# Performance work log

Hardware: AMD Instinct MI355X
Metric: run time of the kernel (lower is better)

Reference implementation:

```python
import jax, jax.numpy as jnp
import numpy as np

N_HEAD = 16
ROPE_BASE = 10000.0


def setup_inputs() -> dict:
    key = jax.random.key(0)
    ks = jax.random.split(key, 5)
    B, T, C = 4, 1024, 2048
    s_in = 1.0 / np.sqrt(C)
    return {
        "x": jax.random.normal(ks[0], (B, T, C), dtype=jnp.float32),
        "w_attn": jax.random.normal(ks[1], (C, 3 * C), dtype=jnp.float32) * s_in,
        "b_attn": jax.random.normal(ks[2], (3 * C,), dtype=jnp.float32) * 0.01,
        "w_proj": jax.random.normal(ks[3], (C, C), dtype=jnp.float32) * s_in,
        "b_proj": jax.random.normal(ks[4], (C,), dtype=jnp.float32) * 0.01,
    }


def _rope(x, cos, sin):
    # x: (B, T, H, D); cos/sin: (T, D//2) -> broadcast over B, H
    d2 = x.shape[-1] // 2
    x1, x2 = x[..., :d2], x[..., d2:]
    c = cos[None, :, None, :]
    s = sin[None, :, None, :]
    return jnp.concatenate([x1 * c - x2 * s, x1 * s + x2 * c], axis=-1)


def reference(x, w_attn, b_attn, w_proj, b_proj):
    B, T, C = x.shape
    H = N_HEAD
    D = C // H
    qkv = (x @ w_attn + b_attn).reshape(B, T, 3, H, D)
    q, k, v = qkv[:, :, 0], qkv[:, :, 1], qkv[:, :, 2]  # (B, T, H, D)

    # Rotary embedding (GPT-NeoX / rotate-half style, full head dim)
    inv_freq = 1.0 / (ROPE_BASE ** (jnp.arange(0, D, 2, dtype=jnp.float32) / D))
    freqs = jnp.arange(T, dtype=jnp.float32)[:, None] * inv_freq[None, :]  # (T, D//2)
    cos, sin = jnp.cos(freqs), jnp.sin(freqs)
    q = _rope(q, cos, sin)
    k = _rope(k, cos, sin)

    scale = 1.0 / jnp.sqrt(jnp.asarray(D, dtype=x.dtype))
    att = jnp.einsum("bqhd,bkhd->bhqk", q, k) * scale  # (B, H, T, T)
    causal = jnp.tril(jnp.ones((T, T), dtype=bool))
    att = jnp.where(causal[None, None], att, jnp.asarray(-jnp.inf, dtype=att.dtype))
    att = jax.nn.softmax(att, axis=-1)
    y = jnp.einsum("bhqk,bkhd->bqhd", att, v).reshape(B, T, C)
    return y @ w_proj + b_proj
```

## Files before the change

kernel.cpp:

```cpp
#include <hip/hip_runtime.h>
#include <math.h>

#define T_SEQ 1024
#define C_DIM 2048
#define H_NUM 16
#define D_HEAD 128
#define BT 4096
#define QKV_N 6144

typedef __bf16 bf16x8 __attribute__((ext_vector_type(8)));
typedef float f32x4 __attribute__((ext_vector_type(4)));
typedef unsigned short u16;
typedef unsigned int u32;

#define AS1C(p) ((const __attribute__((address_space(1))) void*)(p))
#define AS3(p)  ((__attribute__((address_space(3))) void*)(p))

__device__ __forceinline__ u16 f2bf(float f) {
    u32 u = __builtin_bit_cast(u32, f);
    u += 0x7fffu + ((u >> 16) & 1u);
    return (u16)(u >> 16);
}
__device__ __forceinline__ void unpack8(uint4 u, float* f) {
    const u32 w0 = u.x, w1 = u.y, w2 = u.z, w3 = u.w;
    f[0] = __builtin_bit_cast(float, w0 << 16);
    f[1] = __builtin_bit_cast(float, w0 & 0xffff0000u);
    f[2] = __builtin_bit_cast(float, w1 << 16);
    f[3] = __builtin_bit_cast(float, w1 & 0xffff0000u);
    f[4] = __builtin_bit_cast(float, w2 << 16);
    f[5] = __builtin_bit_cast(float, w2 & 0xffff0000u);
    f[6] = __builtin_bit_cast(float, w3 << 16);
    f[7] = __builtin_bit_cast(float, w3 & 0xffff0000u);
}
__device__ __forceinline__ uint4 pack8(const float* f) {
    uint4 u;
    u.x = (u32)f2bf(f[0]) | ((u32)f2bf(f[1]) << 16);
    u.y = (u32)f2bf(f[2]) | ((u32)f2bf(f[3]) << 16);
    u.z = (u32)f2bf(f[4]) | ((u32)f2bf(f[5]) << 16);
    u.w = (u32)f2bf(f[6]) | ((u32)f2bf(f[7]) << 16);
    return u;
}

__global__ __launch_bounds__(256) void cast_bf16(
    const float* __restrict__ in, u16* __restrict__ out)
{
    int i = blockIdx.x * 256 + threadIdx.x;
    float4 v = ((const float4*)in)[i];
    ushort4 o;
    o.x = f2bf(v.x); o.y = f2bf(v.y); o.z = f2bf(v.z); o.w = f2bf(v.w);
    ((ushort4*)out)[i] = o;
}

__global__ __launch_bounds__(256) void transpose_cast(
    const float* __restrict__ in, u16* __restrict__ out, int R, int Cc)
{
    __shared__ float tile[32][33];
    const int c0 = blockIdx.x * 32, r0 = blockIdx.y * 32;
    const int tx = threadIdx.x & 31, ty = threadIdx.x >> 5;
#pragma unroll
    for (int i = 0; i < 32; i += 8)
        tile[ty + i][tx] = in[(size_t)(r0 + ty + i) * Cc + c0 + tx];
    __syncthreads();
#pragma unroll
    for (int i = 0; i < 32; i += 8)
        out[(size_t)(c0 + ty + i) * R + r0 + tx] = f2bf(tile[tx][ty + i]);
}

template <int OUT_BF16>
__global__ __launch_bounds__(512, 2) void gemm_bf16_256(
    const u16* __restrict__ A,
    const u16* __restrict__ Bt,
    const float* __restrict__ bias,
    void* __restrict__ Cout,
    int M, int N, int K)
{
    __shared__ alignas(16) char lds[2][49152];

    const int tid  = threadIdx.x;
    const int lane = tid & 63;
    const int w    = tid >> 6;
    const int wr   = w >> 1;
    const int wc   = w & 1;
    const int l15  = lane & 15;
    const int l4   = lane >> 4;
    const int m0   = blockIdx.y * 256;
    const int n0   = blockIdx.x * 128;
    const int NT   = K >> 6;

    f32x4 acc[4][4] = {};

    const int srow  = w * 16 + (lane >> 3);
    const int sslot = (lane & 7) ^ (lane >> 3);
    const size_t aoff = (size_t)(m0 + srow) * K + sslot * 8;
    const size_t boff = (size_t)(n0 + srow) * K + sslot * 8;
    const int sdst = w * 2048;

    auto stageA = [&](char* buf, int h, int k0) {
#pragma unroll
        for (int i = 0; i < 2; ++i)
            __builtin_amdgcn_global_load_lds(
                AS1C(A + aoff + (size_t)(h * 128 + i * 8) * K + k0),
                AS3(buf + h * 16384 + sdst + i * 1024), 16, 0, 0);
    };
    auto stageB = [&](char* buf, int k0) {
#pragma unroll
        for (int i = 0; i < 2; ++i)
            __builtin_amdgcn_global_load_lds(
                AS1C(Bt + boff + (size_t)(i * 8) * K + k0),
                AS3(buf + 32768 + sdst + i * 1024), 16, 0, 0);
    };

    stageB(lds[0], 0);
    stageA(lds[0], 0, 0);
    stageA(lds[0], 1, 0);
    stageB(lds[1], 64);
    stageA(lds[1], 0, 64);
    asm volatile("s_waitcnt vmcnt(4)" ::: "memory");
    __builtin_amdgcn_s_barrier();

    const int sl0  = (l4 ^ (l15 & 7)) << 4;
    const int sl1  = sl0 ^ 64;
    const int arow = (wr * 32 + l15) * 128;
    const int brow = 32768 + (wc * 64 + l15) * 128;

    for (int kt = 0; kt < NT; ++kt) {
        char* cb = lds[kt & 1];
        char* nb = lds[(kt & 1) ^ 1];

        bf16x8 bfr[4][2], af[2][2];
#pragma unroll
        for (int nt = 0; nt < 4; ++nt) {
            bfr[nt][0] = __builtin_bit_cast(bf16x8,
                *(const uint4*)(cb + brow + nt * 2048 + sl0));
            bfr[nt][1] = __builtin_bit_cast(bf16x8,
                *(const uint4*)(cb + brow + nt * 2048 + sl1));
        }
#pragma unroll
        for (int mt = 0; mt < 2; ++mt) {
            af[mt][0] = __builtin_bit_cast(bf16x8,
                *(const uint4*)(cb + arow + mt * 2048 + sl0));
            af[mt][1] = __builtin_bit_cast(bf16x8,
                *(const uint4*)(cb + arow + mt * 2048 + sl1));
        }
        if (kt + 1 < NT) stageA(nb, 1, (kt + 1) << 6);
        __builtin_amdgcn_s_barrier();
        asm volatile("s_waitcnt lgkmcnt(0)" ::: "memory");
        __builtin_amdgcn_s_setprio(1);
#pragma unroll
        for (int mt = 0; mt < 2; ++mt)
#pragma unroll
            for (int nt = 0; nt < 4; ++nt)
#pragma unroll
                for (int kk = 0; kk < 2; ++kk)
                    acc[mt][nt] = __builtin_amdgcn_mfma_f32_16x16x32_bf16(
                        af[mt][kk], bfr[nt][kk], acc[mt][nt], 0, 0, 0);
        __builtin_amdgcn_s_setprio(0);
        __builtin_amdgcn_s_barrier();

        bf16x8 ag[2][2];
#pragma unroll
        for (int mt = 0; mt < 2; ++mt) {
            ag[mt][0] = __builtin_bit_cast(bf16x8,
                *(const uint4*)(cb + 16384 + arow + mt * 2048 + sl0));
            ag[mt][1] = __builtin_bit_cast(bf16x8,
                *(const uint4*)(cb + 16384 + arow + mt * 2048 + sl1));
        }
        if (kt + 2 < NT) {
            stageB(cb, (kt + 2) << 6);
            stageA(cb, 0, (kt + 2) << 6);
        }
        __builtin_amdgcn_s_barrier();
        asm volatile("s_waitcnt lgkmcnt(0)" ::: "memory");
        __builtin_amdgcn_s_setprio(1);
#pragma unroll
        for (int mt = 0; mt < 2; ++mt)
#pragma unroll
            for (int nt = 0; nt < 4; ++nt)
#pragma unroll
                for (int kk = 0; kk < 2; ++kk)
                    acc[mt + 2][nt] = __builtin_amdgcn_mfma_f32_16x16x32_bf16(
                        ag[mt][kk], bfr[nt][kk], acc[mt + 2][nt], 0, 0, 0);
        __builtin_amdgcn_s_setprio(0);
        if (kt < NT - 2)
            asm volatile("s_waitcnt vmcnt(4)" ::: "memory");
        else
            asm volatile("s_waitcnt vmcnt(0)" ::: "memory");
        __builtin_amdgcn_s_barrier();
    }

#pragma unroll
    for (int nt = 0; nt < 4; ++nt) {
        const int colg = n0 + wc * 64 + nt * 16 + l15;
        const float bv = bias[colg];
#pragma unroll
        for (int mt = 0; mt < 4; ++mt) {
            const int rowb = m0 + (mt < 2 ? wr * 32 + mt * 16
                                          : 128 + wr * 32 + (mt - 2) * 16) + l4 * 4;
#pragma unroll
            for (int r = 0; r < 4; ++r) {
                const float v = acc[mt][nt][r] + bv;
                if (OUT_BF16)
                    ((u16*)Cout)[(size_t)(rowb + r) * N + colg] = f2bf(v);
                else
                    ((float*)Cout)[(size_t)(rowb + r) * N + colg] = v;
            }
        }
    }
}

__global__ __launch_bounds__(256) void rope_table(
    float* __restrict__ ct, float* __restrict__ st)
{
    const int i = blockIdx.x * 256 + threadIdx.x;
    const int d2 = i & 63, t = i >> 6;
    const float invf = expf(-(float)d2 * (9.210340371976184f / 64.0f));
    const float fr = (float)t * invf;
    ct[i] = cosf(fr);
    st[i] = sinf(fr);
}

__global__ __launch_bounds__(256) void rope_kv(
    const u16* __restrict__ qkv, const float* __restrict__ ct,
    const float* __restrict__ st,
    u16* __restrict__ Qc, u16* __restrict__ Kc, u16* __restrict__ Vt)
{
    const int tid = threadIdx.x;
    const int blk = blockIdx.x;
    const int tt = blk & 3;
    const int h  = (blk >> 2) & 15;
    const int b  = blk >> 6;
    const int t  = tt * 256 + tid;
    const int bh = b * 16 + h;

    const size_t src  = ((size_t)(b * T_SEQ + t)) * QKV_N + h * D_HEAD;
    const size_t dst  = ((size_t)(bh * T_SEQ + t)) * D_HEAD;
    const size_t vdst = ((size_t)bh * D_HEAD) * T_SEQ + t;
    const float* crow = ct + t * 64;
    const float* srow = st + t * 64;

#pragma unroll
    for (int part = 0; part < 2; ++part) {
        const u16* in  = qkv + src + part * C_DIM;
        u16* outp      = (part ? Kc : Qc) + dst;
#pragma unroll
        for (int c = 0; c < 8; ++c) {
            uint4 u1 = *(const uint4*)(in + c * 8);
            uint4 u2 = *(const uint4*)(in + 64 + c * 8);
            float f1[8], f2[8], o1[8], o2[8];
            unpack8(u1, f1); unpack8(u2, f2);
#pragma unroll
            for (int i = 0; i < 8; ++i) {
                const float cv = crow[c * 8 + i], sv = srow[c * 8 + i];
                o1[i] = f1[i] * cv - f2[i] * sv;
                o2[i] = f1[i] * sv + f2[i] * cv;
            }
            *(uint4*)(outp + c * 8)      = pack8(o1);
            *(uint4*)(outp + 64 + c * 8) = pack8(o2);
        }
    }

#pragma unroll
    for (int c = 0; c < 16; ++c) {
        uint4 v = *(const uint4*)(qkv + src + 2 * C_DIM + c * 8);
        u16 e[8];
        e[0] = (u16)(v.x & 0xffff); e[1] = (u16)(v.x >> 16);
        e[2] = (u16)(v.y & 0xffff); e[3] = (u16)(v.y >> 16);
        e[4] = (u16)(v.z & 0xffff); e[5] = (u16)(v.z >> 16);
        e[6] = (u16)(v.w & 0xffff); e[7] = (u16)(v.w >> 16);
#pragma unroll
        for (int j = 0; j < 8; ++j)
            Vt[vdst + (size_t)(c * 8 + j) * T_SEQ] = e[j];
    }
}

__global__ __launch_bounds__(256) void attn_mfma(
    const u16* __restrict__ Qc,
    const u16* __restrict__ Kc,
    const u16* __restrict__ Vt,
    u16* __restrict__ y)
{
    __shared__ alignas(16) char KsL[2][16384];
    __shared__ alignas(16) char VtsL[2][16384];
    __shared__ alignas(16) char PwL[4][2176];

    const int tid  = threadIdx.x;
    const int lane = tid & 63;
    const int w    = tid >> 6;
    const int l15  = lane & 15;
    const int l4   = lane >> 4;
    const int p    = blockIdx.x;
    const int bh   = blockIdx.y;
    const int h    = bh & 15;
    const int b    = bh >> 4;

    const size_t kbase = (size_t)bh * T_SEQ * D_HEAD;
    const size_t vbase = (size_t)bh * D_HEAD * T_SEQ;
    const float scale = 0.08838834764831845f;
    char* pw = PwL[w];

    for (int half = 0; half < 2; ++half) {
        const int qt = half ? (15 - p) : p;

        const int qrow = qt * 64 + w * 16 + l15;
        const u16* qptr = Qc + ((size_t)(bh * T_SEQ + qrow)) * D_HEAD;
        bf16x8 qf[4];
#pragma unroll
        for (int f = 0; f < 4; ++f)
            qf[f] = __builtin_bit_cast(bf16x8, *(const uint4*)(qptr + f * 32 + l4 * 8));

        f32x4 o[8] = {};
        float lrow[4] = {};

        __syncthreads();

        {
            const u16* ksrc = Kc + kbase + (size_t)(0 * 64 + lane) * D_HEAD;
#pragma unroll
            for (int i = 0; i < 4; ++i) {
                const int cd = w * 4 + i;
                __builtin_amdgcn_global_load_lds(AS1C(ksrc + cd * 8),
                                                 AS3(KsL[0] + cd * 1024), 16, 0, 0);
            }
#pragma unroll
            for (int i = 0; i < 4; ++i) {
                const int jc = w + (i >> 1) * 4;
                const int dh = i & 1;
                const u16* vsrc = Vt + vbase + (size_t)(dh * 64 + lane) * T_SEQ
                                  + 0 * 64 + jc * 8;
                __builtin_amdgcn_global_load_lds(AS1C(vsrc),
                                                 AS3(VtsL[0] + jc * 2048 + dh * 1024), 16, 0, 0);
            }
        }

        int buf = 0;
        for (int kt = 0; kt <= qt; ++kt, buf ^= 1) {
            __syncthreads();
            if (kt < qt) {
                const int kn = kt + 1;
                char* kb = KsL[buf ^ 1];
                char* vb = VtsL[buf ^ 1];
                const u16* ksrc = Kc + kbase + (size_t)(kn * 64 + lane) * D_HEAD;
#pragma unroll
                for (int i = 0; i < 4; ++i) {
                    const int cd = w * 4 + i;
                    __builtin_amdgcn_global_load_lds(AS1C(ksrc + cd * 8),
                                                     AS3(kb + cd * 1024), 16, 0, 0);
                }
#pragma unroll
                for (int i = 0; i < 4; ++i) {
                    const int jc = w + (i >> 1) * 4;
                    const int dh = i & 1;
                    const u16* vsrc = Vt + vbase + (size_t)(dh * 64 + lane) * T_SEQ
                                      + kn * 64 + jc * 8;
                    __builtin_amdgcn_global_load_lds(AS1C(vsrc),
                                                     AS3(vb + jc * 2048 + dh * 1024), 16, 0, 0);
                }
            }

            const char* kbuf = KsL[buf];
            const char* vbuf = VtsL[buf];

            f32x4 sacc[4] = {};
#pragma unroll
            for (int nb = 0; nb < 4; ++nb)
#pragma unroll
                for (int kc = 0; kc < 4; ++kc) {
                    bf16x8 kf = __builtin_bit_cast(bf16x8,
                        *(const uint4*)(kbuf + (kc * 4 + l4) * 1024 + (nb * 16 + l15) * 16));
                    sacc[nb] = __builtin_amdgcn_mfma_f32_16x16x32_bf16(
                        qf[kc], kf, sacc[nb], 0, 0, 0);
                }

#pragma unroll
            for (int nb = 0; nb < 4; ++nb)
#pragma unroll
                for (int r = 0; r < 4; ++r) {
                    const bool masked =
                        (kt == qt) && ((nb * 16 + l15) > (w * 16 + l4 * 4 + r));
                    const float e = masked ? 0.f
                        : __expf(sacc[nb][r] * scale - 8.0f);
                    sacc[nb][r] = e;
                    lrow[r] += e;
                }

#pragma unroll
            for (int nb = 0; nb < 4; ++nb)
#pragma unroll
                for (int r = 0; r < 4; ++r) {
                    const int j = nb * 16 + l15;
                    const int q = l4 * 4 + r;
                    *(u16*)(pw + (j >> 3) * 272 + q * 16 + (j & 7) * 2) =
                        f2bf(sacc[nb][r]);
                }

            bf16x8 pf[2];
#pragma unroll
            for (int kc2 = 0; kc2 < 2; ++kc2)
                pf[kc2] = __builtin_bit_cast(bf16x8,
                    *(const uint4*)(pw + (kc2 * 4 + l4) * 272 + l15 * 16));
#pragma unroll
            for (int db = 0; db < 8; ++db)
#pragma unroll
                for (int kc2 = 0; kc2 < 2; ++kc2) {
                    bf16x8 vf = __builtin_bit_cast(bf16x8,
                        *(const uint4*)(vbuf + (kc2 * 4 + l4) * 2048 + (db * 16 + l15) * 16));
                    o[db] = __builtin_amdgcn_mfma_f32_16x16x32_bf16(
                        pf[kc2], vf, o[db], 0, 0, 0);
                }
        }

        float inv[4];
#pragma unroll
        for (int r = 0; r < 4; ++r) {
            float ls = lrow[r];
#pragma unroll
            for (int off = 1; off < 16; off <<= 1)
                ls += __shfl_xor(ls, off, 64);
            inv[r] = 1.f / ls;
        }
#pragma unroll
        for (int db = 0; db < 8; ++db)
#pragma unroll
            for (int r = 0; r < 4; ++r) {
                const int q = qt * 64 + w * 16 + l4 * 4 + r;
                const int d = h * D_HEAD + db * 16 + l15;
                y[(size_t)(b * T_SEQ + q) * C_DIM + d] = f2bf(o[db][r] * inv[r]);
            }
    }
}

extern "C" void kernel_launch(void* const* d_in, const int* in_sizes, int n_in,
                              void* d_out, int out_size, void* d_ws, size_t ws_size,
                              hipStream_t stream) {
    const float* x      = (const float*)d_in[0];
    const float* w_attn = (const float*)d_in[1];
    const float* b_attn = (const float*)d_in[2];
    const float* w_proj = (const float*)d_in[3];
    const float* b_proj = (const float*)d_in[4];
    float* out = (float*)d_out;

    char* ws = (char*)d_ws;
    u16* xb   = (u16*)(ws);
    u16* waT  = (u16*)(ws + 16777216);
    u16* Qc   = (u16*)(ws);
    u16* Kc   = (u16*)(ws + 16777216);
    u16* Vt   = (u16*)(ws + 33554432);
    u16* qkvb = (u16*)(ws + 50331648);
    u16* wpT  = (u16*)(ws + 50331648);
    u16* yb   = (u16*)(ws + 100663296);
    float* ct = (float*)(ws + 100663296);
    float* st = ct + 65536;

    cast_bf16<<<(BT * C_DIM / 4) / 256, 256, 0, stream>>>(x, xb);
    transpose_cast<<<dim3(QKV_N / 32, C_DIM / 32), 256, 0, stream>>>(w_attn, waT, C_DIM, QKV_N);
    rope_table<<<(T_SEQ * 64) / 256, 256, 0, stream>>>(ct, st);

    gemm_bf16_256<1><<<dim3(QKV_N / 128, BT / 256), 512, 0, stream>>>(
        xb, waT, b_attn, qkvb, BT, QKV_N, C_DIM);

    rope_kv<<<256, 256, 0, stream>>>(qkvb, ct, st, Qc, Kc, Vt);

    transpose_cast<<<dim3(C_DIM / 32, C_DIM / 32), 256, 0, stream>>>(w_proj, wpT, C_DIM, C_DIM);

    attn_mfma<<<dim3(8, 4 * H_NUM), 256, 0, stream>>>(Qc, Kc, Vt, yb);

    gemm_bf16_256<0><<<dim3(C_DIM / 128, BT / 256), 512, 0, stream>>>(
        yb, wpT, b_proj, out, BT, C_DIM, C_DIM);
}
```

Baseline: 399.7 us.

## Add 256x256 phased-pipeline GEMM for QKV and LDS-staged V transpose

Replaces the QKV projection GEMM with a new 256x256-tile kernel. It interleaves LDS fragment reads, global-to-LDS prefetch and MFMA quads across barrier-separated phases, and uses an XCD-aware 1D block swizzle. The rope_kv kernel now transposes V through a shared-memory tile, so each Vt store is a coalesced 16-byte write instead of a scattered 2-byte one. The bigger tile and 128KB of LDS per block trade occupancy and grid size (384 blocks) for more data reuse and overlap.

```diff
diff --git a/kernel.cpp b/kernel.cpp
--- a/kernel.cpp
+++ b/kernel.cpp
@@ -41,6 +41,16 @@
     return u;
 }
 
+__device__ __forceinline__ void ph_barrier() {
+    asm volatile("" ::: "memory");
+    __builtin_amdgcn_s_barrier();
+    asm volatile("" ::: "memory");
+}
+__device__ __forceinline__ void lgkm0() {
+    asm volatile("s_waitcnt lgkmcnt(0)" ::: "memory");
+    __builtin_amdgcn_sched_barrier(0);
+}
+
 __global__ __launch_bounds__(256) void cast_bf16(
     const float* __restrict__ in, u16* __restrict__ out)
 {
@@ -64,6 +74,144 @@
 #pragma unroll
     for (int i = 0; i < 32; i += 8)
         out[(size_t)(c0 + ty + i) * R + r0 + tx] = f2bf(tile[tx][ty + i]);
+}
+
+template <int OUT_BF16>
+__global__ __launch_bounds__(512, 2) void gemm_bf16_8ph(
+    const u16* __restrict__ A,
+    const u16* __restrict__ Bt,
+    const float* __restrict__ bias,
+    void* __restrict__ Cout,
+    int M, int N, int K, int gx)
+{
+    __shared__ alignas(16) char lds[2][65536];
+
+    const int tid  = threadIdx.x;
+    const int lane = tid & 63;
+    const int w    = tid >> 6;
+    const int wr   = w >> 2;
+    const int wc   = w & 3;
+    const int l15  = lane & 15;
+    const int l4   = lane >> 4;
+
+    const int nwg = gridDim.x;
+    const int cpx = nwg >> 3;
+    const int swz = (blockIdx.x & 7) * cpx + (blockIdx.x >> 3);
+    const int bx  = swz % gx, by = swz / gx;
+    const int m0  = by * 256;
+    const int n0  = bx * 256;
+    const int NT  = K >> 6;
+    const int NI  = NT >> 1;
+
+    f32x4 acc[8][4] = {};
+
+    const int srow  = w * 16 + (lane >> 3);
+    const int sslot = (lane & 7) ^ (lane >> 3);
+    const size_t abase = (size_t)(m0 + srow) * K + sslot * 8;
+    const size_t bbase = (size_t)(n0 + srow) * K + sslot * 8;
+    const int sdst = w * 2048;
+
+    auto stage = [&](char* buf, int mat, int hh, int k0) {
+        const u16* srcp = mat ? Bt : A;
+        const size_t base = mat ? bbase : abase;
+#pragma unroll
+        for (int i = 0; i < 2; ++i)
+            __builtin_amdgcn_global_load_lds(
+                AS1C(srcp + base + (size_t)(hh * 128 + i * 8) * K + k0),
+                AS3(buf + mat * 32768 + hh * 16384 + sdst + i * 1024), 16, 0, 0);
+    };
+
+    const int sl0 = (l4 ^ (l15 & 7)) << 4;
+
+    auto rdA = [&](char* cb, bf16x8 (&afr)[4][2], int mbase) {
+#pragma unroll
+        for (int mt = 0; mt < 4; ++mt) {
+            const int rb = (wr * 128 + (mbase + mt) * 16 + l15) * 128;
+            afr[mt][0] = __builtin_bit_cast(bf16x8, *(const uint4*)(cb + rb + sl0));
+            afr[mt][1] = __builtin_bit_cast(bf16x8, *(const uint4*)(cb + rb + (sl0 ^ 64)));
+        }
+    };
+    auto rdB = [&](char* cb, bf16x8 (&bfr)[4][2], int nbase) {
+#pragma unroll
+        for (int nt = 0; nt < 2; ++nt) {
+            const int rb = 32768 + (wc * 64 + (nbase + nt) * 16 + l15) * 128;
+            bfr[nbase + nt][0] = __builtin_bit_cast(bf16x8, *(const uint4*)(cb + rb + sl0));
+            bfr[nbase + nt][1] = __builtin_bit_cast(bf16x8, *(const uint4*)(cb + rb + (sl0 ^ 64)));
+        }
+    };
+    auto quad = [&](bf16x8 (&afr)[4][2], bf16x8 (&bfr)[4][2], int mb, int nb) {
+        __builtin_amdgcn_s_setprio(1);
+#pragma unroll
+        for (int mt = 0; mt < 4; ++mt)
+#pragma unroll
+            for (int nt = 0; nt < 2; ++nt)
+#pragma unroll
+                for (int kk = 0; kk < 2; ++kk)
+                    acc[mb + mt][nb + nt] = __builtin_amdgcn_mfma_f32_16x16x32_bf16(
+                        afr[mt][kk], bfr[nb + nt][kk], acc[mb + mt][nb + nt], 0, 0, 0);
+        __builtin_amdgcn_s_setprio(0);
+    };
+
+    stage(lds[0], 1, 0, 0);  stage(lds[0], 1, 1, 0);
+    stage(lds[0], 0, 0, 0);  stage(lds[0], 0, 1, 0);
+    stage(lds[1], 1, 0, 64); stage(lds[1], 1, 1, 64);
+    stage(lds[1], 0, 0, 64); stage(lds[1], 0, 1, 64);
+    asm volatile("s_waitcnt vmcnt(8)" ::: "memory");
+    ph_barrier();
+
+    for (int it = 0; it < NI; ++it) {
+        const bool st = (it + 1 < NI);
+#pragma unroll
+        for (int hf = 0; hf < 2; ++hf) {
+            char* cb = lds[hf];
+            const int kS = (2 * it + 2 + hf) << 6;
+            bf16x8 afr[4][2], bfr[4][2];
+
+            rdB(cb, bfr, 0);
+            rdA(cb, afr, 0);
+            ph_barrier(); lgkm0();
+            quad(afr, bfr, 0, 0);
+            ph_barrier();
+
+            rdB(cb, bfr, 2);
+            ph_barrier(); lgkm0();
+            quad(afr, bfr, 0, 2);
+            ph_barrier();
+
+            rdA(cb, afr, 4);
+            if (st) { stage(cb, 1, 0, kS); stage(cb, 1, 1, kS); }
+            ph_barrier(); lgkm0();
+            quad(afr, bfr, 4, 2);
+            ph_barrier();
+
+            if (st) { stage(cb, 0, 0, kS); stage(cb, 0, 1, kS); }
+            ph_barrier();
+            quad(afr, bfr, 4, 0);
+            if (st)
+                asm volatile("s_waitcnt vmcnt(8)" ::: "memory");
+            else if (hf == 0)
+                asm volatile("s_waitcnt vmcnt(0)" ::: "memory");
+            ph_barrier();
+        }
+    }
+
+#pragma unroll
+    for (int nt = 0; nt < 4; ++nt) {
+        const int colg = n0 + wc * 64 + nt * 16 + l15;
+        const float bv = bias[colg];
+#pragma unroll
+        for (int mt = 0; mt < 8; ++mt) {
+            const int rowb = m0 + wr * 128 + mt * 16 + l4 * 4;
+#pragma unroll
+            for (int r = 0; r < 4; ++r) {
+                const float v = acc[mt][nt][r] + bv;
+                if (OUT_BF16)
+                    ((u16*)Cout)[(size_t)(rowb + r) * N + colg] = f2bf(v);
+                else
+                    ((float*)Cout)[(size_t)(rowb + r) * N + colg] = v;
+            }
+        }
+    }
 }
 
 template <int OUT_BF16>
@@ -224,6 +372,7 @@
     const float* __restrict__ st,
     u16* __restrict__ Qc, u16* __restrict__ Kc, u16* __restrict__ Vt)
 {
+    __shared__ u16 vtile[128][264];
     const int tid = threadIdx.x;
     const int blk = blockIdx.x;
     const int tt = blk & 3;
@@ -234,7 +383,6 @@
 
     const size_t src  = ((size_t)(b * T_SEQ + t)) * QKV_N + h * D_HEAD;
     const size_t dst  = ((size_t)(bh * T_SEQ + t)) * D_HEAD;
-    const size_t vdst = ((size_t)bh * D_HEAD) * T_SEQ + t;
     const float* crow = ct + t * 64;
     const float* srow = st + t * 64;
 
@@ -269,7 +417,17 @@
         e[6] = (u16)(v.w & 0xffff); e[7] = (u16)(v.w >> 16);
 #pragma unroll
         for (int j = 0; j < 8; ++j)
-            Vt[vdst + (size_t)(c * 8 + j) * T_SEQ] = e[j];
+            vtile[c * 8 + j][tid] = e[j];
+    }
+    __syncthreads();
+
+    const int dl = tid >> 5;
+    const int jc = (tid & 31) * 8;
+    u16* vt = Vt + ((size_t)bh * D_HEAD) * T_SEQ + (size_t)tt * 256;
+#pragma unroll
+    for (int pass = 0; pass < 16; ++pass) {
+        const int d = pass * 8 + dl;
+        *(uint4*)(vt + (size_t)d * T_SEQ + jc) = *(const uint4*)&vtile[d][jc];
     }
 }
 
@@ -455,8 +613,8 @@
     transpose_cast<<<dim3(QKV_N / 32, C_DIM / 32), 256, 0, stream>>>(w_attn, waT, C_DIM, QKV_N);
     rope_table<<<(T_SEQ * 64) / 256, 256, 0, stream>>>(ct, st);
 
-    gemm_bf16_256<1><<<dim3(QKV_N / 128, BT / 256), 512, 0, stream>>>(
-        xb, waT, b_attn, qkvb, BT, QKV_N, C_DIM);
+    gemm_bf16_8ph<1><<<dim3((QKV_N / 256) * (BT / 256)), 512, 0, stream>>>(
+        xb, waT, b_attn, qkvb, BT, QKV_N, C_DIM, QKV_N / 256);
 
     rope_kv<<<256, 256, 0, stream>>>(qkvb, ct, st, Qc, Kc, Vt);
 
```

New measurement: 415.1 us. 3.9% more time.

## Retile GEMMs to 128xBN blocks, drop barriers, coalesce RoPE and V transpose

Applied to the files above, without the earlier changes.

The GEMM moves from 256x128 tiles to 128xBN tiles (BN=192 for the QKV projection, 128 for the output projection) with a 2x4 wave layout. It asks for 4 blocks per CU and removes the extra barrier plus lgkmcnt waits in each half-step, so more blocks fit on the GPU and compute overlaps with loads better. The RoPE kernel now spreads each row across 16 lanes and pairs the halves with a cross-lane shuffle, and the V transpose goes through an LDS tile so the stores are coalesced. Removing the barriers could open LDS read/write races between phases, and the new tile shape loads more A/B data per flop.

```diff
diff --git a/kernel.cpp b/kernel.cpp
--- a/kernel.cpp
+++ b/kernel.cpp
@@ -41,6 +41,12 @@
     return u;
 }
 
+__device__ __forceinline__ void ph_barrier() {
+    asm volatile("" ::: "memory");
+    __builtin_amdgcn_s_barrier();
+    asm volatile("" ::: "memory");
+}
+
 __global__ __launch_bounds__(256) void cast_bf16(
     const float* __restrict__ in, u16* __restrict__ out)
 {
@@ -66,70 +72,72 @@
         out[(size_t)(c0 + ty + i) * R + r0 + tx] = f2bf(tile[tx][ty + i]);
 }
 
-template <int OUT_BF16>
-__global__ __launch_bounds__(512, 2) void gemm_bf16_256(
+template <int BN, int OUT_BF16>
+__global__ __launch_bounds__(512, 4) void gemm_bf16_ov(
     const u16* __restrict__ A,
     const u16* __restrict__ Bt,
     const float* __restrict__ bias,
     void* __restrict__ Cout,
     int M, int N, int K)
 {
-    __shared__ alignas(16) char lds[2][49152];
+    constexpr int BI  = BN / 64;
+    constexpr int NTW = BN / 64;
+    constexpr int WCOLS = BN / 4;
+    __shared__ alignas(16) char lds[2][16384 + BN * 128];
 
     const int tid  = threadIdx.x;
     const int lane = tid & 63;
     const int w    = tid >> 6;
-    const int wr   = w >> 1;
-    const int wc   = w & 1;
+    const int wr   = w >> 2;
+    const int wc   = w & 3;
     const int l15  = lane & 15;
     const int l4   = lane >> 4;
-    const int m0   = blockIdx.y * 256;
-    const int n0   = blockIdx.x * 128;
+    const int m0   = blockIdx.y * 128;
+    const int n0   = blockIdx.x * BN;
     const int NT   = K >> 6;
 
-    f32x4 acc[4][4] = {};
+    f32x4 acc[4][NTW] = {};
 
     const int srow  = w * 16 + (lane >> 3);
     const int sslot = (lane & 7) ^ (lane >> 3);
     const size_t aoff = (size_t)(m0 + srow) * K + sslot * 8;
-    const size_t boff = (size_t)(n0 + srow) * K + sslot * 8;
-    const int sdst = w * 2048;
-
-    auto stageA = [&](char* buf, int h, int k0) {
+    const int brow_s = w * 8 + (lane >> 3);
+    const size_t boff = (size_t)(n0 + brow_s) * K + sslot * 8;
+
+    auto stageA = [&](char* buf, int k0) {
 #pragma unroll
         for (int i = 0; i < 2; ++i)
             __builtin_amdgcn_global_load_lds(
-                AS1C(A + aoff + (size_t)(h * 128 + i * 8) * K + k0),
-                AS3(buf + h * 16384 + sdst + i * 1024), 16, 0, 0);
+                AS1C(A + aoff + (size_t)(i * 8) * K + k0),
+                AS3(buf + w * 2048 + i * 1024), 16, 0, 0);
     };
     auto stageB = [&](char* buf, int k0) {
 #pragma unroll
-        for (int i = 0; i < 2; ++i)
+        for (int i = 0; i < BI; ++i)
             __builtin_amdgcn_global_load_lds(
-                AS1C(Bt + boff + (size_t)(i * 8) * K + k0),
-                AS3(buf + 32768 + sdst + i * 1024), 16, 0, 0);
+                AS1C(Bt + boff + (size_t)(i * 64) * K + k0),
+                AS3(buf + 16384 + i * 8192 + w * 1024), 16, 0, 0);
     };
 
     stageB(lds[0], 0);
-    stageA(lds[0], 0, 0);
-    stageA(lds[0], 1, 0);
+    stageA(lds[0], 0);
     stageB(lds[1], 64);
-    stageA(lds[1], 0, 64);
-    asm volatile("s_waitcnt vmcnt(4)" ::: "memory");
-    __builtin_amdgcn_s_barrier();
+    if (BI == 3) asm volatile("s_waitcnt vmcnt(3)" ::: "memory");
+    else         asm volatile("s_waitcnt vmcnt(2)" ::: "memory");
+    ph_barrier();
 
     const int sl0  = (l4 ^ (l15 & 7)) << 4;
     const int sl1  = sl0 ^ 64;
-    const int arow = (wr * 32 + l15) * 128;
-    const int brow = 32768 + (wc * 64 + l15) * 128;
+    const int arow = (wr * 64 + l15) * 128;
+    const int brow = 16384 + (wc * WCOLS + l15) * 128;
 
     for (int kt = 0; kt < NT; ++kt) {
         char* cb = lds[kt & 1];
         char* nb = lds[(kt & 1) ^ 1];
 
-        bf16x8 bfr[4][2], af[2][2];
-#pragma unroll
-        for (int nt = 0; nt < 4; ++nt) {
+        bf16x8 bfr[NTW][2], af[2][2];
+#pragma unroll
+        for (int nt = 0; nt < NTW; ++nt) {
             bfr[nt][0] = __builtin_bit_cast(bf16x8,
                 *(const uint4*)(cb + brow + nt * 2048 + sl0));
             bfr[nt][1] = __builtin_bit_cast(bf16x8,
@@ -142,60 +150,54 @@
             af[mt][1] = __builtin_bit_cast(bf16x8,
                 *(const uint4*)(cb + arow + mt * 2048 + sl1));
         }
-        if (kt + 1 < NT) stageA(nb, 1, (kt + 1) << 6);
-        __builtin_amdgcn_s_barrier();
-        asm volatile("s_waitcnt lgkmcnt(0)" ::: "memory");
+        if (kt + 1 < NT) stageA(nb, (kt + 1) << 6);
         __builtin_amdgcn_s_setprio(1);
 #pragma unroll
         for (int mt = 0; mt < 2; ++mt)
 #pragma unroll
-            for (int nt = 0; nt < 4; ++nt)
+            for (int nt = 0; nt < NTW; ++nt)
 #pragma unroll
                 for (int kk = 0; kk < 2; ++kk)
                     acc[mt][nt] = __builtin_amdgcn_mfma_f32_16x16x32_bf16(
                         af[mt][kk], bfr[nt][kk], acc[mt][nt], 0, 0, 0);
         __builtin_amdgcn_s_setprio(0);
-        __builtin_amdgcn_s_barrier();
+        ph_barrier();
 
         bf16x8 ag[2][2];
 #pragma unroll
         for (int mt = 0; mt < 2; ++mt) {
             ag[mt][0] = __builtin_bit_cast(bf16x8,
-                *(const uint4*)(cb + 16384 + arow + mt * 2048 + sl0));
+                *(const uint4*)(cb + arow + (2 + mt) * 2048 + sl0));
             ag[mt][1] = __builtin_bit_cast(bf16x8,
-                *(const uint4*)(cb + 16384 + arow + mt * 2048 + sl1));
-        }
-        if (kt + 2 < NT) {
-            stageB(cb, (kt + 2) << 6);
-            stageA(cb, 0, (kt + 2) << 6);
-        }
-        __builtin_amdgcn_s_barrier();
-        asm volatile("s_waitcnt lgkmcnt(0)" ::: "memory");
+                *(const uint4*)(cb + arow + (2 + mt) * 2048 + sl1));
+        }
+        if (kt + 2 < NT) stageB(cb, (kt + 2) << 6);
         __builtin_amdgcn_s_setprio(1);
 #pragma unroll
         for (int mt = 0; mt < 2; ++mt)
 #pragma unroll
-            for (int nt = 0; nt < 4; ++nt)
+            for (int nt = 0; nt < NTW; ++nt)
 #pragma unroll
                 for (int kk = 0; kk < 2; ++kk)
                     acc[mt + 2][nt] = __builtin_amdgcn_mfma_f32_16x16x32_bf16(
                         ag[mt][kk], bfr[nt][kk], acc[mt + 2][nt], 0, 0, 0);
         __builtin_amdgcn_s_setprio(0);
-        if (kt < NT - 2)
-            asm volatile("s_waitcnt vmcnt(4)" ::: "memory");
-        else
+        if (kt < NT - 2) {
+            if (BI == 3) asm volatile("s_waitcnt vmcnt(3)" ::: "memory");
+            else         asm volatile("s_waitcnt vmcnt(2)" ::: "memory");
+        } else {
             asm volatile("s_waitcnt vmcnt(0)" ::: "memory");
-        __builtin_amdgcn_s_barrier();
-    }
-
-#pragma unroll
-    for (int nt = 0; nt < 4; ++nt) {
-        const int colg = n0 + wc * 64 + nt * 16 + l15;
+        }
+        ph_barrier();
+    }
+
+#pragma unroll
+    for (int nt = 0; nt < NTW; ++nt) {
+        const int colg = n0 + wc * WCOLS + nt * 16 + l15;
         const float bv = bias[colg];
 #pragma unroll
         for (int mt = 0; mt < 4; ++mt) {
-            const int rowb = m0 + (mt < 2 ? wr * 32 + mt * 16
-                                          : 128 + wr * 32 + (mt - 2) * 16) + l4 * 4;
+            const int rowb = m0 + wr * 64 + mt * 16 + l4 * 4;
 #pragma unroll
             for (int r = 0; r < 4; ++r) {
                 const float v = acc[mt][nt][r] + bv;
@@ -224,44 +226,56 @@
     const float* __restrict__ st,
     u16* __restrict__ Qc, u16* __restrict__ Kc, u16* __restrict__ Vt)
 {
+    __shared__ u16 vtile[128][264];
     const int tid = threadIdx.x;
     const int blk = blockIdx.x;
     const int tt = blk & 3;
     const int h  = (blk >> 2) & 15;
     const int b  = blk >> 6;
-    const int t  = tt * 256 + tid;
     const int bh = b * 16 + h;
 
-    const size_t src  = ((size_t)(b * T_SEQ + t)) * QKV_N + h * D_HEAD;
-    const size_t dst  = ((size_t)(bh * T_SEQ + t)) * D_HEAD;
-    const size_t vdst = ((size_t)bh * D_HEAD) * T_SEQ + t;
-    const float* crow = ct + t * 64;
-    const float* srow = st + t * 64;
-
-#pragma unroll
-    for (int part = 0; part < 2; ++part) {
-        const u16* in  = qkv + src + part * C_DIM;
-        u16* outp      = (part ? Kc : Qc) + dst;
-#pragma unroll
-        for (int c = 0; c < 8; ++c) {
-            uint4 u1 = *(const uint4*)(in + c * 8);
-            uint4 u2 = *(const uint4*)(in + 64 + c * 8);
-            float f1[8], f2[8], o1[8], o2[8];
-            unpack8(u1, f1); unpack8(u2, f2);
-#pragma unroll
-            for (int i = 0; i < 8; ++i) {
-                const float cv = crow[c * 8 + i], sv = srow[c * 8 + i];
-                o1[i] = f1[i] * cv - f2[i] * sv;
-                o2[i] = f1[i] * sv + f2[i] * cv;
-            }
-            *(uint4*)(outp + c * 8)      = pack8(o1);
-            *(uint4*)(outp + 64 + c * 8) = pack8(o2);
-        }
-    }
-
+    const int c8 = tid & 15;
+    const int rg = tid >> 4;
+    const float sgn = (c8 < 8) ? -1.f : 1.f;
+
+#pragma unroll 4
+    for (int s = 0; s < 16; ++s) {
+        const int row = s * 16 + rg;
+        const int t   = tt * 256 + row;
+        const size_t rsrc = (size_t)(b * T_SEQ + t) * QKV_N + h * D_HEAD;
+        const size_t rdst = (size_t)(bh * T_SEQ + t) * D_HEAD + c8 * 8;
+
+        const float* crow = ct + t * 64 + (c8 & 7) * 8;
+        const float* srow = st + t * 64 + (c8 & 7) * 8;
+        float cs[8], sn[8];
+        *(float4*)(cs)     = *(const float4*)(crow);
+        *(float4*)(cs + 4) = *(const float4*)(crow + 4);
+        *(float4*)(sn)     = *(const float4*)(srow);
+        *(float4*)(sn + 4) = *(const float4*)(srow + 4);
+
+#pragma unroll
+        for (int part = 0; part < 2; ++part) {
+            uint4 u = *(const uint4*)(qkv + rsrc + part * C_DIM + c8 * 8);
+            uint4 pu;
+            pu.x = (u32)__shfl_xor((int)u.x, 8, 64);
+            pu.y = (u32)__shfl_xor((int)u.y, 8, 64);
+            pu.z = (u32)__shfl_xor((int)u.z, 8, 64);
+            pu.w = (u32)__shfl_xor((int)u.w, 8, 64);
+            float f[8], pf[8], o[8];
+            unpack8(u, f); unpack8(pu, pf);
+#pragma unroll
+            for (int i = 0; i < 8; ++i)
+                o[i] = f[i] * cs[i] + sgn * pf[i] * sn[i];
+            u16* outp = (part ? Kc : Qc) + rdst;
+            *(uint4*)outp = pack8(o);
+        }
+    }
+
+    const int t = tt * 256 + tid;
+    const size_t vsrc = (size_t)(b * T_SEQ + t) * QKV_N + 2 * C_DIM + h * D_HEAD;
 #pragma unroll
     for (int c = 0; c < 16; ++c) {
-        uint4 v = *(const uint4*)(qkv + src + 2 * C_DIM + c * 8);
+        uint4 v = *(const uint4*)(qkv + vsrc + c * 8);
         u16 e[8];
         e[0] = (u16)(v.x & 0xffff); e[1] = (u16)(v.x >> 16);
         e[2] = (u16)(v.y & 0xffff); e[3] = (u16)(v.y >> 16);
@@ -269,7 +283,17 @@
         e[6] = (u16)(v.w & 0xffff); e[7] = (u16)(v.w >> 16);
 #pragma unroll
         for (int j = 0; j < 8; ++j)
-            Vt[vdst + (size_t)(c * 8 + j) * T_SEQ] = e[j];
+            vtile[c * 8 + j][tid] = e[j];
+    }
+    __syncthreads();
+
+    const int dl = tid >> 5;
+    const int jc = (tid & 31) * 8;
+    u16* vt = Vt + ((size_t)bh * D_HEAD) * T_SEQ + (size_t)tt * 256;
+#pragma unroll
+    for (int pass = 0; pass < 16; ++pass) {
+        const int d = pass * 8 + dl;
+        *(uint4*)(vt + (size_t)d * T_SEQ + jc) = *(const uint4*)&vtile[d][jc];
     }
 }
 
@@ -455,7 +479,7 @@
     transpose_cast<<<dim3(QKV_N / 32, C_DIM / 32), 256, 0, stream>>>(w_attn, waT, C_DIM, QKV_N);
     rope_table<<<(T_SEQ * 64) / 256, 256, 0, stream>>>(ct, st);
 
-    gemm_bf16_256<1><<<dim3(QKV_N / 128, BT / 256), 512, 0, stream>>>(
+    gemm_bf16_ov<192, 1><<<dim3(QKV_N / 192, BT / 128), 512, 0, stream>>>(
         xb, waT, b_attn, qkvb, BT, QKV_N, C_DIM);
 
     rope_kv<<<256, 256, 0, stream>>>(qkvb, ct, st, Qc, Kc, Vt);
@@ -464,6 +488,6 @@
 
     attn_mfma<<<dim3(8, 4 * H_NUM), 256, 0, stream>>>(Qc, Kc, Vt, yb);
 
-    gemm_bf16_256<0><<<dim3(C_DIM / 128, BT / 256), 512, 0, stream>>>(
+    gemm_bf16_ov<128, 0><<<dim3(C_DIM / 128, BT / 128), 512, 0, stream>>>(
         yb, wpT, b_proj, out, BT, C_DIM, C_DIM);
 }
```

Measured after the change: 351.2 us. -12.1%, faster.
